# Kernel tuning notes

Hardware: AMD Instinct MI355X
Metric: run time of the kernel (lower is better)

The kernel has to match this reference:

```python
import jax, jax.numpy as jnp
import numpy as np

N_NODES = 100_000
N_EDGES = 3_200_000
D_IN, D_EDGE, D_HID, D_OUT = 8, 4, 32, 16
NEG_SLOPE = 0.2  # PyG GATv2Conv default


def setup_inputs() -> dict:
    key = jax.random.key(0)
    ks = jax.random.split(key, 13)
    s = 0.1
    return {
        "x": jax.random.normal(ks[0], (N_NODES, D_IN), jnp.float32),
        "edge_index": jax.random.randint(ks[1], (2, N_EDGES), 0, N_NODES, dtype=jnp.int64),
        "edge_attr": jax.random.normal(ks[2], (N_EDGES, D_EDGE), jnp.float32),
        "Wl1": jax.random.normal(ks[3], (D_IN, D_HID), jnp.float32) * s,
        "Wr1": jax.random.normal(ks[4], (D_IN, D_HID), jnp.float32) * s,
        "We1": jax.random.normal(ks[5], (D_EDGE, D_HID), jnp.float32) * s,
        "att1": jax.random.normal(ks[6], (D_HID,), jnp.float32) * s,
        "b1": jnp.zeros((D_HID,), jnp.float32),
        "Wl2": jax.random.normal(ks[7], (D_HID, D_OUT), jnp.float32) * s,
        "Wr2": jax.random.normal(ks[8], (D_HID, D_OUT), jnp.float32) * s,
        "We2": jax.random.normal(ks[9], (D_EDGE, D_OUT), jnp.float32) * s,
        "att2": jax.random.normal(ks[10], (D_OUT,), jnp.float32) * s,
        "b2": jnp.zeros((D_OUT,), jnp.float32),
    }


def _segment_softmax(score, seg, n):
    m = jax.ops.segment_max(score, seg, num_segments=n)
    e = jnp.exp(score - m[seg])
    z = jax.ops.segment_sum(e, seg, num_segments=n)
    return e / z[seg]


def _gatv2(x, src, dst, ea_raw, Wl, Wr, We, att, bias, n):
    # GATv2 (heads=1): score_ij = att . leaky_relu(Wl x_j + Wr x_i + We e_ij)
    xl = x @ Wl            # [N, d]
    xr = x @ Wr            # [N, d]
    ea = ea_raw @ We       # [E, d]
    h = jax.nn.leaky_relu(xl[src] + xr[dst] + ea, NEG_SLOPE)  # [E, d]
    score = h @ att        # [E]
    alpha = _segment_softmax(score, dst, n)
    out = jax.ops.segment_sum(alpha[:, None] * xl[src], dst, num_segments=n)
    return out + bias


def reference(x, edge_index, edge_attr, Wl1, Wr1, We1, att1, b1, Wl2, Wr2, We2, att2, b2):
    n = x.shape[0]
    src, dst = edge_index[0], edge_index[1]
    # add_self_loops=True with fill_value='mean': self-loop edge_attr = mean of
    # incoming raw edge_attr per target node (0 for isolated targets)
    ones = jnp.ones((src.shape[0],), x.dtype)
    cnt = jax.ops.segment_sum(ones, dst, num_segments=n)
    loop_attr = jax.ops.segment_sum(edge_attr, dst, num_segments=n) / jnp.maximum(cnt, 1.0)[:, None]
    ar = jnp.arange(n, dtype=src.dtype)
    src2 = jnp.concatenate([src, ar])
    dst2 = jnp.concatenate([dst, ar])
    ea2 = jnp.concatenate([edge_attr, loop_attr], axis=0)
    h = jax.nn.relu(_gatv2(x, src2, dst2, ea2, Wl1, Wr1, We1, att1, b1, n))
    out = _gatv2(h, src2, dst2, ea2, Wl2, Wr2, We2, att2, b2, n)
    return out.reshape(-1)
```

## Files before the change

kernel.cpp:

```cpp
#include <hip/hip_runtime.h>

#define NEG_SLOPE 0.2f
#define CHUNK 16384
#define KMAX  1600
#define CAP   3264
#define NBLKMAX 256

__global__ __launch_bounds__(1024) void k_bin(const int* __restrict__ ei,
                                              const float* __restrict__ eattr,
                                              int* __restrict__ cloff,
                                              int* __restrict__ ssrc,
                                              float4* __restrict__ seat,
                                              int E, int K) {
    __shared__ int s_off[KMAX + 1];
    __shared__ unsigned s_eid[CHUNK];
    int t = threadIdx.x;
    for (int i = t; i <= K; i += 1024) s_off[i] = 0;
    __syncthreads();
    int base = blockIdx.x * CHUNK;
    int end = min(base + CHUNK, E);
    int Ec = end - base;
    unsigned pack[CHUNK / 1024];
#pragma unroll
    for (int i = 0; i < CHUNK / 1024; i++) {
        int el = t + 1024 * i;
        pack[i] = 0xFFFFFFFFu;
        if (el < Ec) {
            int dst = ei[E + base + el];
            int b = dst >> 6;
            int r = atomicAdd(&s_off[b], 1);
            pack[i] = ((unsigned)b << 20) | ((unsigned)(dst & 63) << 14) | (unsigned)r;
        }
    }
    __syncthreads();
    if (t < 64) {
        int run = 0;
        for (int bb = 0; bb < K; bb += 64) {
            int b = bb + t;
            int v = (b < K) ? s_off[b] : 0;
            int x = v;
#pragma unroll
            for (int off = 1; off < 64; off <<= 1) {
                int y = __shfl_up(x, off, 64);
                if (t >= off) x += y;
            }
            if (b < K) s_off[b] = run + x - v;
            run += __shfl(x, 63, 64);
        }
        if (t == 0) s_off[K] = run;
    }
    __syncthreads();
#pragma unroll
    for (int i = 0; i < CHUNK / 1024; i++) {
        int el = t + 1024 * i;
        if (el < Ec) {
            unsigned p = pack[i];
            int b = p >> 20;
            int r = p & 0x3FFF;
            int dl = (p >> 14) & 63;
            s_eid[s_off[b] + r] = ((unsigned)dl << 14) | (unsigned)el;
        }
    }
    __syncthreads();
    for (int pos = t; pos < Ec; pos += 1024) {
        unsigned v = s_eid[pos];
        int el = v & 0x3FFF;
        int dl = v >> 14;
        int e = base + el;
        int src = ei[e];
        float4 a = *(const float4*)(eattr + 4ll * e);
        ssrc[base + pos] = src | (dl << 17);
        seat[base + pos] = a;
    }
    for (int i = t; i <= K; i += 1024)
        cloff[(long long)blockIdx.x * (K + 1) + i] = s_off[i];
}

__global__ void k_transp(const int* __restrict__ in, int* __restrict__ out, int R, int C) {
    __shared__ int tile[32][33];
    int c0 = blockIdx.x * 32, r0 = blockIdx.y * 32;
    int c = c0 + threadIdx.x, r = r0 + threadIdx.y;
    if (r < R && c < C) tile[threadIdx.y][threadIdx.x] = in[(long long)r * C + c];
    __syncthreads();
    int oc = r0 + threadIdx.x, orr = c0 + threadIdx.y;
    if (orr < C && oc < R) out[(long long)orr * R + oc] = tile[threadIdx.x][threadIdx.y];
}

__global__ void k_btot(const int* __restrict__ cloffT, int* __restrict__ bucketTotal,
                       int K, int NBLK) {
    int b = (blockIdx.x * blockDim.x + threadIdx.x) >> 6;
    int lane = threadIdx.x & 63;
    if (b >= K) return;
    const int* r0 = cloffT + (long long)b * NBLK;
    const int* r1 = r0 + NBLK;
    int s = 0;
    for (int c = lane; c < NBLK; c += 64) s += r1[c] - r0[c];
#pragma unroll
    for (int off = 32; off >= 1; off >>= 1) s += __shfl_xor(s, off, 64);
    if (lane == 0) bucketTotal[b] = s;
}

__global__ void k_scanK(const int* __restrict__ bucketTotal, int* __restrict__ slotBase,
                        int* __restrict__ start, int N, int K) {
    __shared__ int s[512];
    int t = threadIdx.x;
    int v[4];
    int sum = 0;
    int base = t * 4;
    for (int j = 0; j < 4; j++) {
        int b = base + j, x = 0;
        if (b < K) { int nb = min(64, N - (b << 6)); x = bucketTotal[b] + nb; }
        v[j] = sum;
        sum += x;
    }
    s[t] = sum;
    __syncthreads();
    for (int off = 1; off < 512; off <<= 1) {
        int x = (t >= off) ? s[t - off] : 0;
        __syncthreads();
        s[t] += x;
        __syncthreads();
    }
    int tb = s[t] - sum;
    for (int j = 0; j < 4; j++) {
        int b = base + j;
        if (b < K) slotBase[b] = tb + v[j];
    }
    if (t == 511) { slotBase[K] = s[511]; start[N] = s[511]; }
}

__global__ __launch_bounds__(512, 8) void k_perm(const int* __restrict__ ssrc,
                                                 const float4* __restrict__ seat,
                                                 const int* __restrict__ cloffT,
                                                 const int* __restrict__ slotBase,
                                                 int* __restrict__ start,
                                                 int* __restrict__ fsrc,
                                                 float4* __restrict__ feat,
                                                 int N, int K, int NBLK) {
    __shared__ int s_pack[CAP];
    __shared__ int s_g[CAP];
    __shared__ int co[NBLKMAX], qq[NBLKMAX + 1], sc[NBLKMAX];
    __shared__ int hist[64], cur[64], lstart[64];
    __shared__ float lsum[64][4];
    int b = blockIdx.x, t = threadIdx.x;
    int nb = min(64, N - (b << 6));
    if (t < 64) {
        hist[t] = 0; cur[t] = 0;
        lsum[t][0] = 0.f; lsum[t][1] = 0.f; lsum[t][2] = 0.f; lsum[t][3] = 0.f;
    }
    const int* r0 = cloffT + (long long)b * NBLK;
    const int* r1 = r0 + NBLK;
    int len = 0;
    if (t < NBLKMAX) {
        if (t < NBLK) { int c0v = r0[t]; len = r1[t] - c0v; co[t] = c0v; }
        sc[t] = (t < NBLK) ? len : 0;
    }
    __syncthreads();
    for (int off = 1; off < NBLKMAX; off <<= 1) {
        int x = 0;
        if (t < NBLKMAX && t >= off) x = sc[t - off];
        __syncthreads();
        if (t < NBLKMAX) sc[t] += x;
        __syncthreads();
    }
    if (t < NBLK) qq[t] = sc[t] - len;
    if (t == NBLKMAX - 1) qq[NBLK] = sc[NBLKMAX - 1];
    __syncthreads();
    int Eb = qq[NBLK];
    for (int i = t; i < Eb; i += 512) {
        int lo2 = 0, hi2 = NBLK;
        while (lo2 + 1 < hi2) { int mid = (lo2 + hi2) >> 1; if (qq[mid] <= i) lo2 = mid; else hi2 = mid; }
        int g = lo2 * CHUNK + co[lo2] + (i - qq[lo2]);
        int p = ssrc[g];
        s_pack[i] = p;
        s_g[i] = g;
        atomicAdd(&hist[(p >> 17) & 63], 1);
    }
    __syncthreads();
    if (t < 64) {
        int v = (t < nb) ? hist[t] + 1 : 0;
        int x = v;
#pragma unroll
        for (int off = 1; off < 64; off <<= 1) {
            int y = __shfl_up(x, off, 64);
            if (t >= off) x += y;
        }
        lstart[t] = x - v;
        if (t < nb) start[(b << 6) + t] = slotBase[b] + lstart[t];
    }
    __syncthreads();
    int lo = slotBase[b];
    for (int i = t; i < Eb; i += 512) {
        int p = s_pack[i];
        int dl = (p >> 17) & 63;
        int src = p & 0x1FFFF;
        int r = atomicAdd(&cur[dl], 1);
        float4 a = seat[s_g[i]];
        long long pos = lo + lstart[dl] + 1 + r;
        fsrc[pos] = src;
        feat[pos] = a;
        atomicAdd(&lsum[dl][0], a.x);
        atomicAdd(&lsum[dl][1], a.y);
        atomicAdd(&lsum[dl][2], a.z);
        atomicAdd(&lsum[dl][3], a.w);
    }
    __syncthreads();
    if (t < nb) {
        float inv = 1.f / fmaxf((float)hist[t], 1.f);
        long long pos = lo + lstart[t];
        fsrc[pos] = (b << 6) + t;
        feat[pos] = make_float4(lsum[t][0] * inv, lsum[t][1] * inv,
                                lsum[t][2] * inv, lsum[t][3] * inv);
    }
}

template <int DIN, int D>
__global__ void k_xform(const float* __restrict__ x, const float* __restrict__ Wl,
                        const float* __restrict__ Wr, float* __restrict__ xl,
                        float* __restrict__ xr, int N) {
    __shared__ float sWl[DIN * D], sWr[DIN * D];
    for (int i = threadIdx.x; i < DIN * D; i += blockDim.x) { sWl[i] = Wl[i]; sWr[i] = Wr[i]; }
    __syncthreads();
    int t = blockIdx.x * blockDim.x + threadIdx.x;
    if (t >= N * D) return;
    int n = t / D, d = t % D;
    const float* xp = x + (long long)n * DIN;
    float sl = 0.f, sr = 0.f;
#pragma unroll
    for (int k = 0; k < DIN; k++) {
        float xv = xp[k];
        sl += xv * sWl[k * D + d];
        sr += xv * sWr[k * D + d];
    }
    xl[t] = sl;
    xr[t] = sr;
}

template <int L>
__device__ __forceinline__ void gat_edge(bool valid, const float4& a, const float4& xlv,
                                         const float4& we0, const float4& we1,
                                         const float4& we2, const float4& we3,
                                         const float4& av, const float4& xrv,
                                         float4& acc, float& z) {
    float4 v;
    v.x = fmaf(a.x, we0.x, xrv.x); v.x = fmaf(a.y, we1.x, v.x);
    v.x = fmaf(a.z, we2.x, v.x);   v.x = fmaf(a.w, we3.x, v.x); v.x += xlv.x;
    v.y = fmaf(a.x, we0.y, xrv.y); v.y = fmaf(a.y, we1.y, v.y);
    v.y = fmaf(a.z, we2.y, v.y);   v.y = fmaf(a.w, we3.y, v.y); v.y += xlv.y;
    v.z = fmaf(a.x, we0.z, xrv.z); v.z = fmaf(a.y, we1.z, v.z);
    v.z = fmaf(a.z, we2.z, v.z);   v.z = fmaf(a.w, we3.z, v.z); v.z += xlv.z;
    v.w = fmaf(a.x, we0.w, xrv.w); v.w = fmaf(a.y, we1.w, v.w);
    v.w = fmaf(a.z, we2.w, v.w);   v.w = fmaf(a.w, we3.w, v.w); v.w += xlv.w;
    v.x = v.x > 0.f ? v.x : NEG_SLOPE * v.x;
    v.y = v.y > 0.f ? v.y : NEG_SLOPE * v.y;
    v.z = v.z > 0.f ? v.z : NEG_SLOPE * v.z;
    v.w = v.w > 0.f ? v.w : NEG_SLOPE * v.w;
    float sc = av.x * v.x + av.y * v.y + av.z * v.z + av.w * v.w;
#pragma unroll
    for (int off = L / 2; off >= 1; off >>= 1) sc += __shfl_xor(sc, off, 64);
    float ev = valid ? __expf(sc) : 0.f;
    z += ev;
    acc.x = fmaf(ev, xlv.x, acc.x);
    acc.y = fmaf(ev, xlv.y, acc.y);
    acc.z = fmaf(ev, xlv.z, acc.z);
    acc.w = fmaf(ev, xlv.w, acc.w);
}

template <int D, bool RELU>
__global__ void k_gat(const int* __restrict__ fsrc,
                      const float4* __restrict__ feat,
                      const int* __restrict__ start,
                      const float* __restrict__ xl, const float* __restrict__ xr,
                      const float* __restrict__ We, const float* __restrict__ att,
                      const float* __restrict__ bias, float* __restrict__ out, int N) {
    constexpr int L = D / 4;
    constexpr int G = 64 / L;
    int w = (blockIdx.x * blockDim.x + threadIdx.x) >> 6;
    int lane = threadIdx.x & 63;
    if (w >= N) return;
    int g = lane / L;
    int j = lane % L;
    int s0 = start[w], s1 = start[w + 1];
    int cnt = s1 - s0;

    const float4 we0 = *(const float4*)(We + 0 * D + 4 * j);
    const float4 we1 = *(const float4*)(We + 1 * D + 4 * j);
    const float4 we2 = *(const float4*)(We + 2 * D + 4 * j);
    const float4 we3 = *(const float4*)(We + 3 * D + 4 * j);
    const float4 av  = *(const float4*)(att + 4 * j);
    const float4 xrv = *(const float4*)(xr + (long long)w * D + 4 * j);

    float4 acc = make_float4(0.f, 0.f, 0.f, 0.f);
    float z = 0.f;

    int nIt = (cnt + G - 1) / G;
    for (int it = 0; it < nIt; it += 2) {
        int o1 = it * G + g;
        int o2 = o1 + G;
        bool v1 = o1 < cnt;
        bool v2 = o2 < cnt;
        int sl1 = s0 + min(o1, cnt - 1);
        int sl2 = s0 + min(o2, cnt - 1);
        int src1 = fsrc[sl1];
        int src2 = fsrc[sl2];
        float4 a1 = feat[sl1];
        float4 a2 = feat[sl2];
        float4 xlv1 = *(const float4*)(xl + (long long)src1 * D + 4 * j);
        float4 xlv2 = *(const float4*)(xl + (long long)src2 * D + 4 * j);
        gat_edge<L>(v1, a1, xlv1, we0, we1, we2, we3, av, xrv, acc, z);
        gat_edge<L>(v2, a2, xlv2, we0, we1, we2, we3, av, xrv, acc, z);
    }

#pragma unroll
    for (int off = 32; off >= L; off >>= 1) {
        acc.x += __shfl_xor(acc.x, off, 64);
        acc.y += __shfl_xor(acc.y, off, 64);
        acc.z += __shfl_xor(acc.z, off, 64);
        acc.w += __shfl_xor(acc.w, off, 64);
        z += __shfl_xor(z, off, 64);
    }

    if (g == 0) {
        float inv = 1.0f / z;
        float4 bv = *(const float4*)(bias + 4 * j);
        float4 o;
        o.x = acc.x * inv + bv.x;
        o.y = acc.y * inv + bv.y;
        o.z = acc.z * inv + bv.z;
        o.w = acc.w * inv + bv.w;
        if (RELU) {
            o.x = fmaxf(o.x, 0.f); o.y = fmaxf(o.y, 0.f);
            o.z = fmaxf(o.z, 0.f); o.w = fmaxf(o.w, 0.f);
        }
        *(float4*)(out + (long long)w * D + 4 * j) = o;
    }
}

extern "C" void kernel_launch(void* const* d_in, const int* in_sizes, int n_in,
                              void* d_out, int out_size, void* d_ws, size_t ws_size,
                              hipStream_t stream) {
    const float* x     = (const float*)d_in[0];
    const int*   ei    = (const int*)d_in[1];
    const float* eattr = (const float*)d_in[2];
    const float* Wl1   = (const float*)d_in[3];
    const float* Wr1   = (const float*)d_in[4];
    const float* We1   = (const float*)d_in[5];
    const float* att1  = (const float*)d_in[6];
    const float* b1    = (const float*)d_in[7];
    const float* Wl2   = (const float*)d_in[8];
    const float* Wr2   = (const float*)d_in[9];
    const float* We2   = (const float*)d_in[10];
    const float* att2  = (const float*)d_in[11];
    const float* b2    = (const float*)d_in[12];

    const int N = in_sizes[0] / 8;
    const int E = in_sizes[1] / 2;
    const int K = (N + 63) >> 6;
    const int NBLK = (E + CHUNK - 1) / CHUNK;

    int* iws = (int*)d_ws;
    size_t o = 0;
    int* bucketTotal = iws + o; o += K;
    int* slotBase    = iws + o; o += K + 1;
    int* start       = iws + o; o += N + 1;
    int* cloff       = iws + o; o += (size_t)NBLK * (K + 1);
    int* cloffT      = iws + o; o += (size_t)(K + 1) * NBLK;
    o = (o + 7) & ~(size_t)7;
    int*    fsrc = (int*)(iws + o);    o += (size_t)(E + N);
    o = (o + 3) & ~(size_t)3;
    float4* feat = (float4*)(iws + o); o += 4ll * (E + N);
    size_t stage = o;
    int*    ssrc = (int*)(iws + o);    o += (size_t)E;
    o = (o + 3) & ~(size_t)3;
    float4* seat = (float4*)(iws + o); o += 4ll * E;
    float* xl = (float*)(iws + stage);
    float* xr = xl + 32ll * N;
    float* h  = xr + 32ll * N;

    const int B = 256;
    auto cdiv = [](long long a, long long b) { return (int)((a + b - 1) / b); };

    k_bin<<<NBLK, 1024, 0, stream>>>(ei, eattr, cloff, ssrc, seat, E, K);
    dim3 tb(32, 32);
    k_transp<<<dim3(cdiv(K + 1, 32), cdiv(NBLK, 32)), tb, 0, stream>>>(cloff, cloffT, NBLK, K + 1);
    k_btot<<<cdiv(64ll * K, B), B, 0, stream>>>(cloffT, bucketTotal, K, NBLK);
    k_scanK<<<1, 512, 0, stream>>>(bucketTotal, slotBase, start, N, K);
    k_perm<<<K, 512, 0, stream>>>(ssrc, seat, cloffT, slotBase, start, fsrc, feat, N, K, NBLK);

    k_xform<8, 32><<<cdiv(32ll * N, B), B, 0, stream>>>(x, Wl1, Wr1, xl, xr, N);
    k_gat<32, true><<<cdiv(N, 4), B, 0, stream>>>(fsrc, feat, start, xl, xr, We1, att1, b1, h, N);

    k_xform<32, 16><<<cdiv(16ll * N, B), B, 0, stream>>>(h, Wl2, Wr2, xl, xr, N);
    k_gat<16, false><<<cdiv(N, 4), B, 0, stream>>>(fsrc, feat, start, xl, xr, We2, att2, b2, (float*)d_out, N);
}
```

Baseline: 497.0 us.

## Sub-bucket edges by source quarter and process GAT in source-range phases

```diff
diff --git a/kernel.cpp b/kernel.cpp
--- a/kernel.cpp
+++ b/kernel.cpp
@@ -5,6 +5,7 @@
 #define KMAX  1600
 #define CAP   3264
 #define NBLKMAX 256
+#define NDB   49
 
 __global__ __launch_bounds__(1024) void k_bin(const int* __restrict__ ei,
                                               const float* __restrict__ eattr,
@@ -101,7 +102,7 @@
 }
 
 __global__ void k_scanK(const int* __restrict__ bucketTotal, int* __restrict__ slotBase,
-                        int* __restrict__ start, int N, int K) {
+                        int* __restrict__ qofs, int N, int K) {
     __shared__ int s[512];
     int t = threadIdx.x;
     int v[4];
@@ -126,26 +127,27 @@
         int b = base + j;
         if (b < K) slotBase[b] = tb + v[j];
     }
-    if (t == 511) { slotBase[K] = s[511]; start[N] = s[511]; }
+    if (t == 511) { slotBase[K] = s[511]; qofs[4ll * N] = s[511]; }
 }
 
 __global__ __launch_bounds__(512, 8) void k_perm(const int* __restrict__ ssrc,
                                                  const float4* __restrict__ seat,
                                                  const int* __restrict__ cloffT,
                                                  const int* __restrict__ slotBase,
-                                                 int* __restrict__ start,
+                                                 int* __restrict__ qofs,
                                                  int* __restrict__ fsrc,
                                                  float4* __restrict__ feat,
-                                                 int N, int K, int NBLK) {
+                                                 int N, int K, int NBLK, int QDIV) {
     __shared__ int s_pack[CAP];
     __shared__ int s_g[CAP];
     __shared__ int co[NBLKMAX], qq[NBLKMAX + 1], sc[NBLKMAX];
-    __shared__ int hist[64], cur[64], lstart[64];
+    __shared__ int hist2[256], cur2[256], lst2[256], sc2[256];
+    __shared__ int hist[64];
     __shared__ float lsum[64][4];
     int b = blockIdx.x, t = threadIdx.x;
     int nb = min(64, N - (b << 6));
+    if (t < 256) { hist2[t] = 0; cur2[t] = 0; }
     if (t < 64) {
-        hist[t] = 0; cur[t] = 0;
         lsum[t][0] = 0.f; lsum[t][1] = 0.f; lsum[t][2] = 0.f; lsum[t][3] = 0.f;
     }
     const int* r0 = cloffT + (long long)b * NBLK;
@@ -172,32 +174,51 @@
         while (lo2 + 1 < hi2) { int mid = (lo2 + hi2) >> 1; if (qq[mid] <= i) lo2 = mid; else hi2 = mid; }
         int g = lo2 * CHUNK + co[lo2] + (i - qq[lo2]);
         int p = ssrc[g];
-        s_pack[i] = p;
+        int srcv = p & 0x1FFFF;
+        int q = (unsigned)srcv / (unsigned)QDIV;
+        s_pack[i] = p | (q << 23);
         s_g[i] = g;
-        atomicAdd(&hist[(p >> 17) & 63], 1);
+        atomicAdd(&hist2[(((p >> 17) & 63) << 2) | q], 1);
     }
     __syncthreads();
     if (t < 64) {
-        int v = (t < nb) ? hist[t] + 1 : 0;
-        int x = v;
-#pragma unroll
-        for (int off = 1; off < 64; off <<= 1) {
-            int y = __shfl_up(x, off, 64);
-            if (t >= off) x += y;
-        }
-        lstart[t] = x - v;
-        if (t < nb) start[(b << 6) + t] = slotBase[b] + lstart[t];
-    }
+        int c = hist2[4 * t] + hist2[4 * t + 1] + hist2[4 * t + 2] + hist2[4 * t + 3];
+        hist[t] = c;
+        if (t < nb) {
+            int node = (b << 6) + t;
+            int qs = (unsigned)node / (unsigned)QDIV;
+            hist2[t * 4 + qs] += 1;
+            cur2[t * 4 + qs] = 1;
+        }
+    }
+    __syncthreads();
+    if (t < 256) sc2[t] = hist2[t];
+    __syncthreads();
+    for (int off = 1; off < 256; off <<= 1) {
+        int x = 0;
+        if (t < 256 && t >= off) x = sc2[t - off];
+        __syncthreads();
+        if (t < 256) sc2[t] += x;
+        __syncthreads();
+    }
+    if (t < 256) lst2[t] = sc2[t] - hist2[t];
     __syncthreads();
     int lo = slotBase[b];
+    if (t < 256) {
+        int dl = t >> 2;
+        if (dl < nb)
+            qofs[(((long long)((b << 6) + dl)) << 2) + (t & 3)] = lo + lst2[t];
+    }
     for (int i = t; i < Eb; i += 512) {
         int p = s_pack[i];
         int dl = (p >> 17) & 63;
-        int src = p & 0x1FFFF;
-        int r = atomicAdd(&cur[dl], 1);
+        int q = (p >> 23) & 3;
+        int srcv = p & 0x1FFFF;
+        int bin = (dl << 2) | q;
+        int r = atomicAdd(&cur2[bin], 1);
         float4 a = seat[s_g[i]];
-        long long pos = lo + lstart[dl] + 1 + r;
-        fsrc[pos] = src;
+        long long pos = lo + lst2[bin] + r;
+        fsrc[pos] = srcv;
         feat[pos] = a;
         atomicAdd(&lsum[dl][0], a.x);
         atomicAdd(&lsum[dl][1], a.y);
@@ -206,9 +227,11 @@
     }
     __syncthreads();
     if (t < nb) {
+        int node = (b << 6) + t;
+        int qs = (unsigned)node / (unsigned)QDIV;
         float inv = 1.f / fmaxf((float)hist[t], 1.f);
-        long long pos = lo + lstart[t];
-        fsrc[pos] = (b << 6) + t;
+        long long pos = lo + lst2[t * 4 + qs];
+        fsrc[pos] = node;
         feat[pos] = make_float4(lsum[t][0] * inv, lsum[t][1] * inv,
                                 lsum[t][2] * inv, lsum[t][3] * inv);
     }
@@ -266,73 +289,88 @@
     acc.w = fmaf(ev, xlv.w, acc.w);
 }
 
-template <int D, bool RELU>
-__global__ void k_gat(const int* __restrict__ fsrc,
+template <int D, int NPHASE, bool RELU>
+__global__ __launch_bounds__(256, 8) void k_gat(const int* __restrict__ fsrc,
                       const float4* __restrict__ feat,
-                      const int* __restrict__ start,
+                      const int* __restrict__ qofs,
                       const float* __restrict__ xl, const float* __restrict__ xr,
                       const float* __restrict__ We, const float* __restrict__ att,
                       const float* __restrict__ bias, float* __restrict__ out, int N) {
     constexpr int L = D / 4;
     constexpr int G = 64 / L;
-    int w = (blockIdx.x * blockDim.x + threadIdx.x) >> 6;
-    int lane = threadIdx.x & 63;
-    if (w >= N) return;
+    __shared__ float part[NDB][D + 4];
+    __shared__ float xrl[NDB][D];
+    int d0 = blockIdx.x * NDB;
+    int nd = min(NDB, N - d0);
+    int tid = threadIdx.x;
+    for (int i = tid; i < nd * D; i += 256) xrl[i / D][i % D] = xr[(long long)d0 * D + i];
+    for (int i = tid; i < nd * (D + 4); i += 256) part[i / (D + 4)][i % (D + 4)] = 0.f;
+    __syncthreads();
+    int wv = tid >> 6;
+    int lane = tid & 63;
     int g = lane / L;
     int j = lane % L;
-    int s0 = start[w], s1 = start[w + 1];
-    int cnt = s1 - s0;
 
     const float4 we0 = *(const float4*)(We + 0 * D + 4 * j);
     const float4 we1 = *(const float4*)(We + 1 * D + 4 * j);
     const float4 we2 = *(const float4*)(We + 2 * D + 4 * j);
     const float4 we3 = *(const float4*)(We + 3 * D + 4 * j);
     const float4 av  = *(const float4*)(att + 4 * j);
-    const float4 xrv = *(const float4*)(xr + (long long)w * D + 4 * j);
-
-    float4 acc = make_float4(0.f, 0.f, 0.f, 0.f);
-    float z = 0.f;
-
-    int nIt = (cnt + G - 1) / G;
-    for (int it = 0; it < nIt; it += 2) {
-        int o1 = it * G + g;
-        int o2 = o1 + G;
-        bool v1 = o1 < cnt;
-        bool v2 = o2 < cnt;
-        int sl1 = s0 + min(o1, cnt - 1);
-        int sl2 = s0 + min(o2, cnt - 1);
-        int src1 = fsrc[sl1];
-        int src2 = fsrc[sl2];
-        float4 a1 = feat[sl1];
-        float4 a2 = feat[sl2];
-        float4 xlv1 = *(const float4*)(xl + (long long)src1 * D + 4 * j);
-        float4 xlv2 = *(const float4*)(xl + (long long)src2 * D + 4 * j);
-        gat_edge<L>(v1, a1, xlv1, we0, we1, we2, we3, av, xrv, acc, z);
-        gat_edge<L>(v2, a2, xlv2, we0, we1, we2, we3, av, xrv, acc, z);
-    }
-
-#pragma unroll
-    for (int off = 32; off >= L; off >>= 1) {
-        acc.x += __shfl_xor(acc.x, off, 64);
-        acc.y += __shfl_xor(acc.y, off, 64);
-        acc.z += __shfl_xor(acc.z, off, 64);
-        acc.w += __shfl_xor(acc.w, off, 64);
-        z += __shfl_xor(z, off, 64);
-    }
-
-    if (g == 0) {
-        float inv = 1.0f / z;
-        float4 bv = *(const float4*)(bias + 4 * j);
-        float4 o;
-        o.x = acc.x * inv + bv.x;
-        o.y = acc.y * inv + bv.y;
-        o.z = acc.z * inv + bv.z;
-        o.w = acc.w * inv + bv.w;
-        if (RELU) {
-            o.x = fmaxf(o.x, 0.f); o.y = fmaxf(o.y, 0.f);
-            o.z = fmaxf(o.z, 0.f); o.w = fmaxf(o.w, 0.f);
-        }
-        *(float4*)(out + (long long)w * D + 4 * j) = o;
+
+    for (int ph = 0; ph < NPHASE; ++ph) {
+        int qlo = (4 * ph) / NPHASE;
+        int qhi = (4 * (ph + 1)) / NPHASE;
+        for (int ld = wv; ld < nd; ld += 4) {
+            int d = d0 + ld;
+            int s0 = qofs[4 * d + qlo];
+            int s1 = qofs[4 * d + qhi];
+            int cnt = s1 - s0;
+            if (cnt == 0) continue;
+            float4 xrv = *(const float4*)&xrl[ld][4 * j];
+            float4 acc = make_float4(0.f, 0.f, 0.f, 0.f);
+            float z = 0.f;
+            for (int it = 0; it * G < cnt; ++it) {
+                int o = it * G + g;
+                bool val = o < cnt;
+                int sl = s0 + min(o, cnt - 1);
+                int src = fsrc[sl];
+                float4 a = feat[sl];
+                float4 xlv = *(const float4*)(xl + (long long)src * D + 4 * j);
+                gat_edge<L>(val, a, xlv, we0, we1, we2, we3, av, xrv, acc, z);
+            }
+#pragma unroll
+            for (int off = 32; off >= L; off >>= 1) {
+                acc.x += __shfl_xor(acc.x, off, 64);
+                acc.y += __shfl_xor(acc.y, off, 64);
+                acc.z += __shfl_xor(acc.z, off, 64);
+                acc.w += __shfl_xor(acc.w, off, 64);
+                z += __shfl_xor(z, off, 64);
+            }
+            if (g == 0) {
+                float4* pp = (float4*)&part[ld][4 * j];
+                float4 cp = *pp;
+                cp.x += acc.x; cp.y += acc.y; cp.z += acc.z; cp.w += acc.w;
+                *pp = cp;
+                if (j == 0) part[ld][D] += z;
+            }
+        }
+    }
+    for (int ld = wv; ld < nd; ld += 4) {
+        if (g == 0) {
+            float inv = 1.f / part[ld][D];
+            float4 nm = *(float4*)&part[ld][4 * j];
+            float4 bv = *(const float4*)(bias + 4 * j);
+            float4 o4;
+            o4.x = nm.x * inv + bv.x;
+            o4.y = nm.y * inv + bv.y;
+            o4.z = nm.z * inv + bv.z;
+            o4.w = nm.w * inv + bv.w;
+            if (RELU) {
+                o4.x = fmaxf(o4.x, 0.f); o4.y = fmaxf(o4.y, 0.f);
+                o4.z = fmaxf(o4.z, 0.f); o4.w = fmaxf(o4.w, 0.f);
+            }
+            *(float4*)(out + (long long)(d0 + ld) * D + 4 * j) = o4;
+        }
     }
 }
 
@@ -357,12 +395,13 @@
     const int E = in_sizes[1] / 2;
     const int K = (N + 63) >> 6;
     const int NBLK = (E + CHUNK - 1) / CHUNK;
+    const int QDIV = (N + 3) / 4;
 
     int* iws = (int*)d_ws;
     size_t o = 0;
     int* bucketTotal = iws + o; o += K;
     int* slotBase    = iws + o; o += K + 1;
-    int* start       = iws + o; o += N + 1;
+    int* qofs        = iws + o; o += 4ll * N + 1;
     int* cloff       = iws + o; o += (size_t)NBLK * (K + 1);
     int* cloffT      = iws + o; o += (size_t)(K + 1) * NBLK;
     o = (o + 7) & ~(size_t)7;
@@ -384,12 +423,14 @@
     dim3 tb(32, 32);
     k_transp<<<dim3(cdiv(K + 1, 32), cdiv(NBLK, 32)), tb, 0, stream>>>(cloff, cloffT, NBLK, K + 1);
     k_btot<<<cdiv(64ll * K, B), B, 0, stream>>>(cloffT, bucketTotal, K, NBLK);
-    k_scanK<<<1, 512, 0, stream>>>(bucketTotal, slotBase, start, N, K);
-    k_perm<<<K, 512, 0, stream>>>(ssrc, seat, cloffT, slotBase, start, fsrc, feat, N, K, NBLK);
+    k_scanK<<<1, 512, 0, stream>>>(bucketTotal, slotBase, qofs, N, K);
+    k_perm<<<K, 512, 0, stream>>>(ssrc, seat, cloffT, slotBase, qofs, fsrc, feat, N, K, NBLK, QDIV);
+
+    const int GGRID = cdiv(N, NDB);
 
     k_xform<8, 32><<<cdiv(32ll * N, B), B, 0, stream>>>(x, Wl1, Wr1, xl, xr, N);
-    k_gat<32, true><<<cdiv(N, 4), B, 0, stream>>>(fsrc, feat, start, xl, xr, We1, att1, b1, h, N);
+    k_gat<32, 4, true><<<GGRID, B, 0, stream>>>(fsrc, feat, qofs, xl, xr, We1, att1, b1, h, N);
 
     k_xform<32, 16><<<cdiv(16ll * N, B), B, 0, stream>>>(h, Wl2, Wr2, xl, xr, N);
-    k_gat<16, false><<<cdiv(N, 4), B, 0, stream>>>(fsrc, feat, start, xl, xr, We2, att2, b2, (float*)d_out, N);
-}
+    k_gat<16, 2, false><<<GGRID, B, 0, stream>>>(fsrc, feat, qofs, xl, xr, We2, att2, b2, (float*)d_out, N);
+}
```

After: 554.6 us. 1.12x slower.
